# Kernel tuning notes

Hardware: AMD Instinct MI355X
Metric: run time of the kernel (lower is better)

Reference implementation:

```python
import jax, jax.numpy as jnp
import numpy as np
from jax import lax

FPS_NUM, K = 2048, 32


def fps_subsample(x, n):
    # x: [B, N, 3] -> [B, n, 3]; farthest point sampling, deterministic start at index 0
    B, N, _ = x.shape
    d0 = jnp.sum((x - x[:, :1]) ** 2, axis=-1)  # [B, N] dist to point 0

    def step(dists, _):
        nxt = jnp.argmax(dists, axis=1)                       # [B]
        p = x[jnp.arange(B), nxt]                             # [B, 3]
        dists = jnp.minimum(dists, jnp.sum((x - p[:, None]) ** 2, axis=-1))
        return dists, nxt

    _, idxs = lax.scan(step, d0, None, length=n - 1)          # [n-1, B]
    idxs = jnp.concatenate([jnp.zeros((1, B), jnp.int32), idxs.astype(jnp.int32)], axis=0).T  # [B, n]
    return x[jnp.arange(B)[:, None], idxs]                    # [B, n, 3]


def knn_idx(x, k):
    # x: [B, C, N] -> [B, N, k] indices of k nearest neighbors in feature space
    xx = jnp.sum(x * x, axis=1)                               # [B, N]
    inner = jnp.einsum('bcn,bcm->bnm', x, x)
    neg_dist = 2.0 * inner - xx[:, :, None] - xx[:, None, :]  # -||xi-xj||^2
    return lax.top_k(neg_dist, k)[1]


def get_graph_feature(x, k):
    # DGCNN edge features: x [B, C, N] -> [B, 2C, N, k]
    B, C, N = x.shape
    idx = knn_idx(x, k)                                       # [B, N, k]
    xt = jnp.transpose(x, (0, 2, 1))                          # [B, N, C]
    nbr = xt[jnp.arange(B)[:, None, None], idx]               # [B, N, k, C]
    ctr = jnp.broadcast_to(xt[:, :, None], nbr.shape)
    feat = jnp.concatenate([nbr - ctr, ctr], axis=-1)         # [B, N, k, 2C]
    return jnp.transpose(feat, (0, 3, 1, 2))


def attention(xq, xk, pos, Wq, bq, Wk, bk, Wv, bv, Wp, bp):
    # positional attention over k neighbors: xq/xk [B, Cin, N, k], pos [B, 3, N] -> [B, dim, N]
    q = jnp.einsum('bcnk,dc->bdnk', xq, Wq) + bq[:, None, None]
    kk = jnp.einsum('bcnk,dc->bdnk', xk, Wk) + bk[:, None, None]
    v = jnp.einsum('bcnk,dc->bdnk', xk, Wv) + bv[:, None, None]
    p = jnp.einsum('bcn,dc->bdn', pos, Wp) + bp[:, None]      # [B, dim, N]
    dim = Wq.shape[0]
    logits = jnp.einsum('bdnk,bdnk->bnk', q, kk) / jnp.sqrt(jnp.float32(dim))
    attn = jax.nn.softmax(logits, axis=-1)                    # [B, N, k]
    return jnp.einsum('bnk,bdnk->bdn', attn, v + p[:, :, :, None])


def _layer_params(key, cin, dim):
    ks = jax.random.split(key, 4)
    s = 1.0 / np.sqrt(cin)
    return (jax.random.normal(ks[0], (dim, cin), jnp.float32) * s,
            jnp.zeros((dim,), jnp.float32),
            jax.random.normal(ks[1], (dim, cin), jnp.float32) * s,
            jnp.zeros((dim,), jnp.float32),
            jax.random.normal(ks[2], (dim, cin), jnp.float32) * s,
            jnp.zeros((dim,), jnp.float32),
            jax.random.normal(ks[3], (dim, 3), jnp.float32) * (1.0 / np.sqrt(3.0)),
            jnp.zeros((dim,), jnp.float32))


def setup_inputs() -> dict:
    key = jax.random.key(0)
    kx, k1, k2, k3 = jax.random.split(key, 4)
    x = jax.random.normal(kx, (8, 16384, 3), jnp.float32)
    out = {'x': x}
    for name, kk_, cin, dim in (('t1', k1, 6, 64), ('t2', k2, 128, 64), ('t3', k3, 128, 128)):
        Wq, bq, Wk, bk, Wv, bv, Wp, bp = _layer_params(kk_, cin, dim)
        out.update({f'{name}_Wq': Wq, f'{name}_bq': bq, f'{name}_Wk': Wk, f'{name}_bk': bk,
                    f'{name}_Wv': Wv, f'{name}_bv': bv, f'{name}_Wp': Wp, f'{name}_bp': bp})
    return out


def reference(x, t1_Wq, t1_bq, t1_Wk, t1_bk, t1_Wv, t1_bv, t1_Wp, t1_bp,
              t2_Wq, t2_bq, t2_Wk, t2_bk, t2_Wv, t2_bv, t2_Wp, t2_bp,
              t3_Wq, t3_bq, t3_Wk, t3_bk, t3_Wv, t3_bv, t3_Wp, t3_bp):
    partial = jnp.transpose(fps_subsample(x, FPS_NUM), (0, 2, 1))       # [B, 3, n]
    g = get_graph_feature(partial, K)                                    # [B, 6, n, k]
    x1 = attention(g, g, partial, t1_Wq, t1_bq, t1_Wk, t1_bk, t1_Wv, t1_bv, t1_Wp, t1_bp)  # [B, 64, n]
    g = get_graph_feature(x1, K)                                         # [B, 128, n, k]
    x2 = attention(g, g, partial, t2_Wq, t2_bq, t2_Wk, t2_bk, t2_Wv, t2_bv, t2_Wp, t2_bp)  # [B, 64, n]
    g = get_graph_feature(x2, K)                                         # [B, 128, n, k]
    x3 = attention(g, g, partial, t3_Wq, t3_bq, t3_Wk, t3_bk, t3_Wv, t3_bv, t3_Wp, t3_bp)  # [B, 128, n]
    feats = jnp.concatenate([x1, x2, x3], axis=1)                        # [B, 256, n]
    return jnp.concatenate([jnp.max(feats, axis=-1), jnp.mean(feats, axis=-1)], axis=1)    # [B, 512]
```

## Files before the change

kernel.cpp:

```cpp
#include <hip/hip_runtime.h>
#include <math.h>

#define NB 8
#define NIN 16384
#define NP 2048
#define KNN 32
#define TOTPTS (NB * NP)

#define NEG_INF (-__builtin_inff())
#define POS_INF (__builtin_inff())

__device__ __forceinline__ float2 pk_add(float2 a, float2 b) {
  float2 d;
  asm("v_pk_add_f32 %0, %1, %2" : "=v"(d) : "v"(a), "v"(b));
  return d;
}
__device__ __forceinline__ float2 pk_mul(float2 a, float2 b) {
  float2 d;
  asm("v_pk_mul_f32 %0, %1, %2" : "=v"(d) : "v"(a), "v"(b));
  return d;
}

#define DPP_F(old, v, C, RM) \
  __int_as_float(__builtin_amdgcn_update_dpp(__float_as_int(old), __float_as_int(v), C, RM, 0xf, false))
#define DPP_I(old, v, C, RM) \
  __builtin_amdgcn_update_dpp(old, v, C, RM, 0xf, false)

__device__ __forceinline__ float wave_max_f(float v) {
  v = fmaxf(v, DPP_F(NEG_INF, v, 0x111, 0xf));
  v = fmaxf(v, DPP_F(NEG_INF, v, 0x112, 0xf));
  v = fmaxf(v, DPP_F(NEG_INF, v, 0x114, 0xf));
  v = fmaxf(v, DPP_F(NEG_INF, v, 0x118, 0xf));
  v = fmaxf(v, DPP_F(NEG_INF, v, 0x142, 0xa));
  v = fmaxf(v, DPP_F(NEG_INF, v, 0x143, 0xc));
  return v;
}
__device__ __forceinline__ float wave_min_f(float v) {
  v = fminf(v, DPP_F(POS_INF, v, 0x111, 0xf));
  v = fminf(v, DPP_F(POS_INF, v, 0x112, 0xf));
  v = fminf(v, DPP_F(POS_INF, v, 0x114, 0xf));
  v = fminf(v, DPP_F(POS_INF, v, 0x118, 0xf));
  v = fminf(v, DPP_F(POS_INF, v, 0x142, 0xa));
  v = fminf(v, DPP_F(POS_INF, v, 0x143, 0xc));
  return v;
}
__device__ __forceinline__ int wave_min_i(int v) {
  v = min(v, DPP_I(0x7fffffff, v, 0x111, 0xf));
  v = min(v, DPP_I(0x7fffffff, v, 0x112, 0xf));
  v = min(v, DPP_I(0x7fffffff, v, 0x114, 0xf));
  v = min(v, DPP_I(0x7fffffff, v, 0x118, 0xf));
  v = min(v, DPP_I(0x7fffffff, v, 0x142, 0xa));
  v = min(v, DPP_I(0x7fffffff, v, 0x143, 0xc));
  return v;
}

template <int CTRL, int RMASK>
__device__ __forceinline__ void dpp_amax_step(float& bv, int& bi) {
  float ov = DPP_F(NEG_INF, bv, CTRL, RMASK);
  int oi = DPP_I(0, bi, CTRL, RMASK);
  if (ov > bv || (ov == bv && oi < bi)) { bv = ov; bi = oi; }
}
__device__ __forceinline__ void wave_amax63(float& bv, int& bi) {
  dpp_amax_step<0x111, 0xf>(bv, bi);
  dpp_amax_step<0x112, 0xf>(bv, bi);
  dpp_amax_step<0x114, 0xf>(bv, bi);
  dpp_amax_step<0x118, 0xf>(bv, bi);
  dpp_amax_step<0x142, 0xa>(bv, bi);
  dpp_amax_step<0x143, 0xc>(bv, bi);
}

__device__ __forceinline__ float readlane63f(float v) {
  return __int_as_float(__builtin_amdgcn_readlane(__float_as_int(v), 63));
}

__device__ __forceinline__ unsigned f2ord(float f) {
  unsigned b = __float_as_uint(f);
  return (b & 0x80000000u) ? ~b : (b | 0x80000000u);
}
__device__ __forceinline__ float ord2f(unsigned u) {
  return __uint_as_float((u & 0x80000000u) ? (u ^ 0x80000000u) : ~u);
}
__device__ __forceinline__ unsigned spread3(unsigned v) {
  return (v & 1u) | ((v & 2u) << 2) | ((v & 4u) << 4) | ((v & 8u) << 6) |
         ((v & 16u) << 8) | ((v & 32u) << 10);
}

__global__ __launch_bounds__(1024) void sort_kernel(const float* __restrict__ x,
                                                    unsigned* __restrict__ ord) {
  const int b = blockIdx.x, t = threadIdx.x;
  const float* xb = x + (size_t)b * NIN * 3;
  __shared__ unsigned keys[NIN];
  __shared__ unsigned smn[3], smx[3];
  if (t < 3) { smn[t] = 0xFFFFFFFFu; smx[t] = 0u; }
  __syncthreads();
  float cx[16], cy[16], cz[16];
  float mnx = POS_INF, mny = POS_INF, mnz = POS_INF;
  float mxx = NEG_INF, mxy = NEG_INF, mxz = NEG_INF;
#pragma unroll
  for (int s = 0; s < 16; ++s) {
    const int i = s * 1024 + t;
    cx[s] = xb[3 * i]; cy[s] = xb[3 * i + 1]; cz[s] = xb[3 * i + 2];
    mnx = fminf(mnx, cx[s]); mxx = fmaxf(mxx, cx[s]);
    mny = fminf(mny, cy[s]); mxy = fmaxf(mxy, cy[s]);
    mnz = fminf(mnz, cz[s]); mxz = fmaxf(mxz, cz[s]);
  }
  mnx = wave_min_f(mnx); mxx = wave_max_f(mxx);
  mny = wave_min_f(mny); mxy = wave_max_f(mxy);
  mnz = wave_min_f(mnz); mxz = wave_max_f(mxz);
  if ((t & 63) == 63) {
    atomicMin(&smn[0], f2ord(mnx)); atomicMax(&smx[0], f2ord(mxx));
    atomicMin(&smn[1], f2ord(mny)); atomicMax(&smx[1], f2ord(mxy));
    atomicMin(&smn[2], f2ord(mnz)); atomicMax(&smx[2], f2ord(mxz));
  }
  __syncthreads();
  const float bx = ord2f(smn[0]), by = ord2f(smn[1]), bz = ord2f(smn[2]);
  const float fx = 63.9f / fmaxf(ord2f(smx[0]) - bx, 1e-30f);
  const float fy = 63.9f / fmaxf(ord2f(smx[1]) - by, 1e-30f);
  const float fz = 63.9f / fmaxf(ord2f(smx[2]) - bz, 1e-30f);
#pragma unroll
  for (int s = 0; s < 16; ++s) {
    const int i = s * 1024 + t;
    const unsigned a0 = min(63u, (unsigned)(int)fmaxf((cx[s] - bx) * fx, 0.f));
    const unsigned a1 = min(63u, (unsigned)(int)fmaxf((cy[s] - by) * fy, 0.f));
    const unsigned a2 = min(63u, (unsigned)(int)fmaxf((cz[s] - bz) * fz, 0.f));
    const unsigned code = spread3(a0) | (spread3(a1) << 1) | (spread3(a2) << 2);
    keys[i] = (code << 14) | (unsigned)i;
  }
  __syncthreads();
  for (unsigned k = 2; k <= (unsigned)NIN; k <<= 1) {
    for (unsigned j = k >> 1; j; j >>= 1) {
#pragma unroll
      for (int s = 0; s < 8; ++s) {
        const unsigned idx = (unsigned)t + (unsigned)s * 1024u;
        const unsigned e = ((idx & ~(j - 1u)) << 1) | (idx & (j - 1u));
        const unsigned p = e | j;
        const unsigned a = keys[e], c = keys[p];
        if ((a > c) == ((e & k) == 0u)) { keys[e] = c; keys[p] = a; }
      }
      __syncthreads();
    }
  }
#pragma unroll
  for (int s = 0; s < 16; ++s) {
    const int i = s * 1024 + t;
    ord[(size_t)b * NIN + i] = keys[i] & 0x3FFFu;
  }
}

#define FPS_UPD(j)                                                            \
  {                                                                           \
    float2 dx = pk_add(px[j], nx2), dy = pk_add(py[j], ny2), dz = pk_add(pz[j], nz2); \
    float2 nd = pk_add(pk_add(pk_mul(dx, dx), pk_mul(dy, dy)), pk_mul(dz, dz));        \
    dd[j].x = fminf(dd[j].x, nd.x);                                           \
    dd[j].y = fminf(dd[j].y, nd.y);                                           \
  }

__global__ __launch_bounds__(1024) void fps_kernel(const float* __restrict__ x,
                                                   const unsigned* __restrict__ ord,
                                                   float* __restrict__ partial) {
  const int b = blockIdx.x;
  const int t = threadIdx.x;
  const int w = t >> 6, l = t & 63;
  const float* xb = x + (size_t)b * NIN * 3;
  float* pb = partial + (size_t)b * NP * 3;
  __shared__ unsigned long long skey[NP];
  for (int i = t; i < NP; i += 1024) skey[i] = 0ull;

  float2 px[8], py[8], pz[8], dd[8];
  int id0[8], id1[8];
  const unsigned* ob = ord + (size_t)b * NIN;
#pragma unroll
  for (int j = 0; j < 8; ++j) {
    const int p0 = ((w * 8 + j) << 7) + l * 2;
    const int g0 = (int)ob[p0], g1 = (int)ob[p0 + 1];
    id0[j] = g0; id1[j] = g1;
    px[j] = make_float2(xb[3 * g0], xb[3 * g1]);
    py[j] = make_float2(xb[3 * g0 + 1], xb[3 * g1 + 1]);
    pz[j] = make_float2(xb[3 * g0 + 2], xb[3 * g1 + 2]);
  }

  float ccx = 0.f, ccy = 0.f, ccz = 0.f, ccr = 0.f;
#pragma unroll
  for (int j = 0; j < 8; ++j) {
    float mnx = wave_min_f(fminf(px[j].x, px[j].y));
    float mxx = wave_max_f(fmaxf(px[j].x, px[j].y));
    float mny = wave_min_f(fminf(py[j].x, py[j].y));
    float mxy = wave_max_f(fmaxf(py[j].x, py[j].y));
    float mnz = wave_min_f(fminf(pz[j].x, pz[j].y));
    float mxz = wave_max_f(fmaxf(pz[j].x, pz[j].y));
    const float cx = 0.5f * (readlane63f(mnx) + readlane63f(mxx));
    const float cy = 0.5f * (readlane63f(mny) + readlane63f(mxy));
    const float cz = 0.5f * (readlane63f(mnz) + readlane63f(mxz));
    float d0x = px[j].x - cx, d0y = py[j].x - cy, d0z = pz[j].x - cz;
    float d1x = px[j].y - cx, d1y = py[j].y - cy, d1z = pz[j].y - cz;
    float d2 = fmaxf(d0x * d0x + d0y * d0y + d0z * d0z,
                     d1x * d1x + d1y * d1y + d1z * d1z);
    d2 = wave_max_f(d2);
    const float r = sqrtf(readlane63f(d2)) * 1.00002f;
    if (l == j) { ccx = cx; ccy = cy; ccz = cz; ccr = r; }
  }

  const float qx0 = xb[0], qy0 = xb[1], qz0 = xb[2];
  if (t == 0) { pb[0] = qx0; pb[1] = qy0; pb[2] = qz0; }

  float bv = NEG_INF;
  int bi = 0x7fffffff;
  {
    const float2 nx2 = make_float2(-qx0, -qx0);
    const float2 ny2 = make_float2(-qy0, -qy0);
    const float2 nz2 = make_float2(-qz0, -qz0);
#pragma unroll
    for (int j = 0; j < 8; ++j) {
      float2 dx = pk_add(px[j], nx2), dy = pk_add(py[j], ny2), dz = pk_add(pz[j], nz2);
      float2 nd = pk_add(pk_add(pk_mul(dx, dx), pk_mul(dy, dy)), pk_mul(dz, dz));
      dd[j] = nd;
      if (nd.x > bv || (nd.x == bv && id0[j] < bi)) { bv = nd.x; bi = id0[j]; }
      if (nd.y > bv || (nd.y == bv && id1[j] < bi)) { bv = nd.y; bi = id1[j]; }
    }
  }
  __syncthreads();

  for (int it = 1; it < NP; ++it) {
    const float wm = wave_max_f(bv);
    const float smaxw = readlane63f(wm);
    const int sel = (bv == smaxw) ? bi : 0x7fffffff;
    const int wi = wave_min_i(sel);
    if (l == 63) {
      const unsigned long long key =
          ((unsigned long long)__float_as_uint(smaxw) << 32) | (unsigned)(~wi);
      atomicMax(&skey[it], key);
    }
    __syncthreads();
    const unsigned long long gk = skey[it];
    const float smax = __uint_as_float((unsigned)(gk >> 32));
    const int u = __builtin_amdgcn_readfirstlane((int)(~(unsigned)gk));
    const float nqx = xb[3 * u], nqy = xb[3 * u + 1], nqz = xb[3 * u + 2];
    if (t == 0) { pb[3 * it] = nqx; pb[3 * it + 1] = nqy; pb[3 * it + 2] = nqz; }

    const float rho = sqrtf(smax) * 1.00002f;
    const float cdx = ccx - nqx, cdy = ccy - nqy, cdz = ccz - nqz;
    const float dq = sqrtf(cdx * cdx + cdy * cdy + cdz * cdz);
    const bool upd = (l < 8) && (dq * 0.99998f < ccr + rho);
    const unsigned m8 = (unsigned)__ballot(upd) & 255u;
    if (m8) {
      const float2 nx2 = make_float2(-nqx, -nqx);
      const float2 ny2 = make_float2(-nqy, -nqy);
      const float2 nz2 = make_float2(-nqz, -nqz);
      if (m8 & 1u) FPS_UPD(0)
      if (m8 & 2u) FPS_UPD(1)
      if (m8 & 4u) FPS_UPD(2)
      if (m8 & 8u) FPS_UPD(3)
      if (m8 & 16u) FPS_UPD(4)
      if (m8 & 32u) FPS_UPD(5)
      if (m8 & 64u) FPS_UPD(6)
      if (m8 & 128u) FPS_UPD(7)
      bv = NEG_INF;
      bi = 0x7fffffff;
#pragma unroll
      for (int j = 0; j < 8; ++j) {
        if (dd[j].x > bv || (dd[j].x == bv && id0[j] < bi)) { bv = dd[j].x; bi = id0[j]; }
        if (dd[j].y > bv || (dd[j].y == bv && id1[j] < bi)) { bv = dd[j].y; bi = id1[j]; }
      }
    }
  }
}

__global__ void xx_kernel(const float* __restrict__ F, float* __restrict__ xxg, int C) {
  int i = blockIdx.x * 256 + threadIdx.x;
  if (i >= TOTPTS) return;
  const float* f = F + (size_t)i * C;
  float s = 0.f;
  for (int c = 0; c < C; ++c) s = __fadd_rn(s, __fmul_rn(f[c], f[c]));
  xxg[i] = s;
}

template <int C>
__global__ __launch_bounds__(256) void dist_gemm(const float* __restrict__ F,
                                                 const float* __restrict__ xxg,
                                                 float* __restrict__ D, int bofs) {
  __shared__ float As[64][C + 1];
  __shared__ float Bs[64][C + 1];
  const int b = bofs + blockIdx.z;
  float* Ds = D + (size_t)blockIdx.z * NP * NP;
  const int tid = threadIdx.x;
  const int n0 = blockIdx.y * 64, m0 = blockIdx.x * 64;
  const float* Fb = F + (size_t)b * NP * C;
  const float* xxb = xxg + b * NP;
  for (int t = tid; t < 64 * C; t += 256) {
    int r = t / C, c = t - r * C;
    As[r][c] = Fb[(size_t)(n0 + r) * C + c];
    Bs[r][c] = Fb[(size_t)(m0 + r) * C + c];
  }
  __syncthreads();
  const int tx = tid & 15, ty = tid >> 4;
  float acc[4][4] = {};
  for (int c = 0; c < C; ++c) {
    float a[4], bb[4];
#pragma unroll
    for (int i = 0; i < 4; ++i) a[i] = As[ty * 4 + i][c];
#pragma unroll
    for (int j = 0; j < 4; ++j) bb[j] = Bs[tx * 4 + j][c];
#pragma unroll
    for (int i = 0; i < 4; ++i)
#pragma unroll
      for (int j = 0; j < 4; ++j) acc[i][j] = fmaf(a[i], bb[j], acc[i][j]);
  }
#pragma unroll
  for (int i = 0; i < 4; ++i) {
    int n = n0 + ty * 4 + i;
    float xn = xxb[n];
    float4 o;
    o.x = __fsub_rn(__fsub_rn(2.0f * acc[i][0], xn), xxb[m0 + tx * 4 + 0]);
    o.y = __fsub_rn(__fsub_rn(2.0f * acc[i][1], xn), xxb[m0 + tx * 4 + 1]);
    o.z = __fsub_rn(__fsub_rn(2.0f * acc[i][2], xn), xxb[m0 + tx * 4 + 2]);
    o.w = __fsub_rn(__fsub_rn(2.0f * acc[i][3], xn), xxb[m0 + tx * 4 + 3]);
    *(float4*)&Ds[(size_t)n * NP + m0 + tx * 4] = o;
  }
}

__global__ __launch_bounds__(256) void select_kernel(const float* __restrict__ D,
                                                     int* __restrict__ idxg, int bofs) {
  const int lane = threadIdx.x & 63;
  const int b = bofs + blockIdx.z;
  const int row = blockIdx.x * 4 + (threadIdx.x >> 6);
  const float* Drow = D + (size_t)blockIdx.z * NP * NP + (size_t)row * NP;
  float v[32];
#pragma unroll
  for (int s = 0; s < 32; ++s) v[s] = Drow[s * 64 + lane];
  int* out = idxg + ((size_t)b * NP + row) * KNN;
  for (int t = 0; t < KNN; ++t) {
    float bv = v[0];
    int bs = 0;
#pragma unroll
    for (int s = 1; s < 32; ++s) {
      if (v[s] > bv) { bv = v[s]; bs = s; }
    }
    int bi = bs * 64 + lane;
    wave_amax63(bv, bi);
    const int wbi = __builtin_amdgcn_readlane(bi, 63);
    if (lane == 0) out[t] = wbi;
    const bool own = (lane == (wbi & 63));
    const int cs = wbi >> 6;
#pragma unroll
    for (int s = 0; s < 32; ++s)
      if (own && s == cs) v[s] = NEG_INF;
  }
}

template <int C, int DIM>
__global__ __launch_bounds__(256) void proj_kernel(
    const float* __restrict__ F, const float* __restrict__ pos,
    const float* __restrict__ Wq, const float* __restrict__ bq,
    const float* __restrict__ Wk, const float* __restrict__ bk,
    const float* __restrict__ Wv, const float* __restrict__ bv,
    const float* __restrict__ Wp, const float* __restrict__ bp,
    float* __restrict__ Uq, float* __restrict__ Uk, float* __restrict__ Uv,
    float* __restrict__ Uqc, float* __restrict__ Ukc, float* __restrict__ W6) {
  constexpr int PTS = 16;
  constexpr int GROUPS = 256 / DIM;
  constexpr int PPT = PTS / GROUPS;
  __shared__ float xs[PTS][C];
  __shared__ float ps[PTS][3];
  const int tid = threadIdx.x;
  const int base = blockIdx.x * PTS;
  for (int t = tid; t < PTS * C; t += 256) {
    int r = t / C;
    xs[r][t - r * C] = F[(size_t)(base + r) * C + (t - r * C)];
  }
  for (int t = tid; t < PTS * 3; t += 256) {
    int r = t / 3;
    ps[r][t - r * 3] = pos[(size_t)(base + r) * 3 + (t - r * 3)];
  }
  __syncthreads();
  const int g = tid / DIM;
  const int d = tid - g * DIM;
  float uq[PPT], uqd[PPT], uk[PPT], ukd[PPT], uv[PPT], uvd[PPT];
#pragma unroll
  for (int p = 0; p < PPT; ++p) { uq[p] = uqd[p] = uk[p] = ukd[p] = uv[p] = uvd[p] = 0.f; }
  const float* wqr = Wq + (size_t)d * (2 * C);
  const float* wkr = Wk + (size_t)d * (2 * C);
  const float* wvr = Wv + (size_t)d * (2 * C);
  for (int c = 0; c < C; ++c) {
    const float wq1 = wqr[c], wqd_ = wqr[C + c] - wq1;
    const float wk1 = wkr[c], wkd_ = wkr[C + c] - wk1;
    const float wv1 = wvr[c], wvd_ = wvr[C + c] - wv1;
#pragma unroll
    for (int p = 0; p < PPT; ++p) {
      const float xc = xs[g + p * GROUPS][c];
      uq[p] = fmaf(wq1, xc, uq[p]);
      uqd[p] = fmaf(wqd_, xc, uqd[p]);
      uk[p] = fmaf(wk1, xc, uk[p]);
      ukd[p] = fmaf(wkd_, xc, ukd[p]);
      uv[p] = fmaf(wv1, xc, uv[p]);
      uvd[p] = fmaf(wvd_, xc, uvd[p]);
    }
  }
  const float bqd = bq[d], bkd = bk[d], bvd = bv[d];
  const float wp0 = Wp[d * 3], wp1 = Wp[d * 3 + 1], wp2 = Wp[d * 3 + 2], bpd = bp[d];
#pragma unroll
  for (int p = 0; p < PPT; ++p) {
    const int lp = g + p * GROUPS;
    const size_t o = (size_t)(base + lp) * DIM + d;
    const float pd = wp0 * ps[lp][0] + wp1 * ps[lp][1] + wp2 * ps[lp][2] + bpd;
    Uq[o] = uq[p];
    Uqc[o] = uqd[p] + bqd;
    Uk[o] = uk[p];
    Ukc[o] = ukd[p] + bkd;
    Uv[o] = uv[p];
    W6[o] = uvd[p] + bvd + pd;
  }
}

template <int DIM>
__global__ void prep_kernel(const float* __restrict__ Wq, const float* __restrict__ bq,
                            const float* __restrict__ Wk, const float* __restrict__ bk,
                            const float* __restrict__ Wv, const float* __restrict__ bv,
                            float* __restrict__ Wcat, float* __restrict__ bcat) {
  const int o = blockIdx.x * 256 + threadIdx.x;
  constexpr int ND = 6 * DIM;
  if (o >= ND) return;
  const int blk = o / DIM, d = o % DIM;
  bcat[o] = (blk == 1) ? bq[d] : (blk == 3) ? bk[d] : (blk == 5) ? bv[d] : 0.f;
  const float* W = (blk < 2) ? Wq : (blk < 4) ? Wk : Wv;
  for (int c = 0; c < 64; ++c) {
    const float w1 = W[(size_t)d * 128 + c];
    const float w2 = W[(size_t)d * 128 + 64 + c];
    Wcat[(size_t)c * ND + o] = (blk & 1) ? (w2 - w1) : w1;
  }
}

template <int DIM>
__global__ void pos_kernel(const float* __restrict__ pos, const float* __restrict__ Wp,
                           const float* __restrict__ bp, float* __restrict__ P) {
  const int idx = blockIdx.x * 256 + threadIdx.x;
  const int pt = idx / DIM, d = idx - pt * DIM;
  P[idx] = Wp[d * 3] * pos[pt * 3] + Wp[d * 3 + 1] * pos[pt * 3 + 1] +
           Wp[d * 3 + 2] * pos[pt * 3 + 2] + bp[d];
}

template <int DIM>
__global__ __launch_bounds__(256) void gemm_proj(
    const float* __restrict__ F, const float* __restrict__ Wcat,
    const float* __restrict__ bcat, const float* __restrict__ P,
    float* __restrict__ Uq, float* __restrict__ Uqc, float* __restrict__ Uk,
    float* __restrict__ Ukc, float* __restrict__ Uv, float* __restrict__ W6) {
  constexpr int ND = 6 * DIM;
  __shared__ float As[64][65];
  __shared__ float Bs[64][65];
  const int tid = threadIdx.x;
  const int p0 = blockIdx.x * 64;
  const int n0 = blockIdx.y * 64;
  {
    const int r0 = tid >> 4, c4 = (tid & 15) * 4;
    for (int r = r0; r < 64; r += 16) {
      float4 a = *(const float4*)&F[(size_t)(p0 + r) * 64 + c4];
      As[r][c4] = a.x; As[r][c4 + 1] = a.y; As[r][c4 + 2] = a.z; As[r][c4 + 3] = a.w;
      float4 bb = *(const float4*)&Wcat[(size_t)r * ND + n0 + c4];
      Bs[r][c4] = bb.x; Bs[r][c4 + 1] = bb.y; Bs[r][c4 + 2] = bb.z; Bs[r][c4 + 3] = bb.w;
    }
  }
  __syncthreads();
  const int tx = tid & 15, ty = tid >> 4;
  float acc[4][4] = {};
#pragma unroll 4
  for (int c = 0; c < 64; ++c) {
    float a[4], bb[4];
#pragma unroll
    for (int i = 0; i < 4; ++i) a[i] = As[ty * 4 + i][c];
#pragma unroll
    for (int j = 0; j < 4; ++j) bb[j] = Bs[c][tx * 4 + j];
#pragma unroll
    for (int i = 0; i < 4; ++i)
#pragma unroll
      for (int j = 0; j < 4; ++j) acc[i][j] = fmaf(a[i], bb[j], acc[i][j]);
  }
  const int obuf = n0 / DIM;
  const int oloc = n0 - obuf * DIM;
  float* outp = (obuf == 0) ? Uq : (obuf == 1) ? Uqc : (obuf == 2) ? Uk
              : (obuf == 3) ? Ukc : (obuf == 4) ? Uv : W6;
  const float b0 = bcat[n0 + tx * 4], b1 = bcat[n0 + tx * 4 + 1];
  const float b2 = bcat[n0 + tx * 4 + 2], b3 = bcat[n0 + tx * 4 + 3];
#pragma unroll
  for (int i = 0; i < 4; ++i) {
    const int p = p0 + ty * 4 + i;
    float4 r = make_float4(acc[i][0] + b0, acc[i][1] + b1, acc[i][2] + b2, acc[i][3] + b3);
    if (obuf == 5) {
      float4 pv = *(const float4*)&P[(size_t)p * DIM + oloc + tx * 4];
      r.x += pv.x; r.y += pv.y; r.z += pv.z; r.w += pv.w;
    }
    *(float4*)&outp[(size_t)p * DIM + oloc + tx * 4] = r;
  }
}

template <int DIM>
__global__ __launch_bounds__(256) void attn_kernel(
    const float* __restrict__ Uq, const float* __restrict__ Uk, const float* __restrict__ Uv,
    const float* __restrict__ Uqc, const float* __restrict__ Ukc, const float* __restrict__ W6g,
    const int* __restrict__ idxg, float* __restrict__ outF) {
  const int w = threadIdx.x >> 6, lane = threadIdx.x & 63;
  const int pt = blockIdx.x * 4 + w;
  const int b = pt >> 11;
  __shared__ int sidx[4][KNN];
  __shared__ float sqc[4][DIM], skc[4][DIM], sw6[4][DIM];
  __shared__ float sattn[4][KNN];
  const size_t rowo = (size_t)pt * DIM;
  if (lane < KNN) sidx[w][lane] = idxg[(size_t)pt * KNN + lane];
  for (int d = lane; d < DIM; d += 64) {
    sqc[w][d] = Uqc[rowo + d];
    skc[w][d] = Ukc[rowo + d];
    sw6[w][d] = W6g[rowo + d];
  }
  __syncthreads();
  {
    const int kk = lane & 31;
    const int h = lane >> 5;
    const int ik = sidx[w][kk];
    const float* qr = Uq + (size_t)(b * NP + ik) * DIM;
    const float* kr = Uk + (size_t)(b * NP + ik) * DIM;
    float lg = 0.f;
    const int d0 = h * (DIM / 2), d1 = d0 + DIM / 2;
    for (int d = d0; d < d1; d += 4) {
      float4 qa = *(const float4*)(qr + d);
      float4 ka = *(const float4*)(kr + d);
      float4 qc = *(const float4*)(&sqc[w][d]);
      float4 kc = *(const float4*)(&skc[w][d]);
      lg += (qa.x + qc.x) * (ka.x + kc.x);
      lg += (qa.y + qc.y) * (ka.y + kc.y);
      lg += (qa.z + qc.z) * (ka.z + kc.z);
      lg += (qa.w + qc.w) * (ka.w + kc.w);
    }
    lg += __shfl_xor(lg, 32);
    lg *= (DIM == 64) ? 0.125f : 0.08838834764831845f;
    float m = lg;
#pragma unroll
    for (int off = 16; off; off >>= 1) m = fmaxf(m, __shfl_xor(m, off));
    float e = expf(lg - m);
    float s = e;
#pragma unroll
    for (int off = 16; off; off >>= 1) s += __shfl_xor(s, off);
    if (lane < KNN) sattn[w][lane] = e / s;
  }
  __syncthreads();
  float acc[DIM / 64];
#pragma unroll
  for (int q = 0; q < DIM / 64; ++q) acc[q] = 0.f;
  for (int k = 0; k < KNN; ++k) {
    const int ik = sidx[w][k];
    const float a = sattn[w][k];
    const float* vr = Uv + (size_t)(b * NP + ik) * DIM;
#pragma unroll
    for (int q = 0; q < DIM / 64; ++q) {
      const int d = q * 64 + lane;
      acc[q] = fmaf(a, vr[d] + sw6[w][d], acc[q]);
    }
  }
#pragma unroll
  for (int q = 0; q < DIM / 64; ++q) outF[rowo + q * 64 + lane] = acc[q];
}

__global__ __launch_bounds__(256) void pool_kernel(const float* __restrict__ x1,
                                                   const float* __restrict__ x2,
                                                   const float* __restrict__ x3,
                                                   float* __restrict__ out) {
  const int b = blockIdx.x, c = threadIdx.x;
  const float* src;
  int dim, cl;
  if (c < 64) {
    src = x1 + (size_t)b * NP * 64; dim = 64; cl = c;
  } else if (c < 128) {
    src = x2 + (size_t)b * NP * 64; dim = 64; cl = c - 64;
  } else {
    src = x3 + (size_t)b * NP * 128; dim = 128; cl = c - 128;
  }
  float mx = NEG_INF, sm = 0.f;
#pragma unroll 8
  for (int n = 0; n < NP; ++n) {
    float v = src[(size_t)n * dim + cl];
    mx = fmaxf(mx, v);
    sm += v;
  }
  out[b * 512 + c] = mx;
  out[b * 512 + 256 + c] = sm * (1.0f / 2048.0f);
}

extern "C" void kernel_launch(void* const* d_in, const int* in_sizes, int n_in,
                              void* d_out, int out_size, void* d_ws, size_t ws_size,
                              hipStream_t stream) {
  const float* x = (const float*)d_in[0];
  const float* W[24];
  for (int i = 0; i < 24; ++i) W[i] = (const float*)d_in[1 + i];

  float* ws = (float*)d_ws;
  size_t off = 0;
  float* partial = ws + off; off += (size_t)NB * NP * 3;
  float* xxbuf = ws + off;   off += TOTPTS;
  int* idxb = (int*)(ws + off); off += (size_t)TOTPTS * KNN;
  unsigned* ordb = (unsigned*)(ws + off); off += (size_t)NB * NIN;
  float* x1 = ws + off; off += (size_t)TOTPTS * 64;
  float* x2 = ws + off; off += (size_t)TOTPTS * 64;
  float* x3 = ws + off; off += (size_t)TOTPTS * 128;
  float* Uq = ws + off;  off += (size_t)TOTPTS * 128;
  float* Uk = ws + off;  off += (size_t)TOTPTS * 128;
  float* Uv = ws + off;  off += (size_t)TOTPTS * 128;
  float* Uqc = ws + off; off += (size_t)TOTPTS * 128;
  float* Ukc = ws + off; off += (size_t)TOTPTS * 128;
  float* W6 = ws + off;  off += (size_t)TOTPTS * 128;
  float* Pbuf = ws + off; off += (size_t)TOTPTS * 128;
  float* Wcat = ws + off; off += (size_t)64 * 768;
  float* bcat = ws + off; off += 768;
  if (ws_size < off * sizeof(float)) return;

  float* Dbig = ws + off;
  const size_t need_big = (off + (size_t)NB * NP * NP) * sizeof(float);
  const bool bigws = (ws_size >= need_big);
  float* D = bigws ? Dbig : Uq;
  const int NZ = bigws ? NB : 1;

  sort_kernel<<<NB, 1024, 0, stream>>>(x, ordb);
  fps_kernel<<<NB, 1024, 0, stream>>>(x, ordb, partial);

  xx_kernel<<<TOTPTS / 256, 256, 0, stream>>>(partial, xxbuf, 3);
  for (int b = 0; b < NB; b += NZ) {
    dist_gemm<3><<<dim3(32, 32, NZ), 256, 0, stream>>>(partial, xxbuf, D, b);
    select_kernel<<<dim3(NP / 4, 1, NZ), 256, 0, stream>>>(D, idxb, b);
  }
  proj_kernel<3, 64><<<TOTPTS / 16, 256, 0, stream>>>(
      partial, partial, W[0], W[1], W[2], W[3], W[4], W[5], W[6], W[7],
      Uq, Uk, Uv, Uqc, Ukc, W6);
  attn_kernel<64><<<TOTPTS / 4, 256, 0, stream>>>(Uq, Uk, Uv, Uqc, Ukc, W6, idxb, x1);

  xx_kernel<<<TOTPTS / 256, 256, 0, stream>>>(x1, xxbuf, 64);
  for (int b = 0; b < NB; b += NZ) {
    dist_gemm<64><<<dim3(32, 32, NZ), 256, 0, stream>>>(x1, xxbuf, D, b);
    select_kernel<<<dim3(NP / 4, 1, NZ), 256, 0, stream>>>(D, idxb, b);
  }
  prep_kernel<64><<<2, 256, 0, stream>>>(W[8], W[9], W[10], W[11], W[12], W[13], Wcat, bcat);
  pos_kernel<64><<<TOTPTS * 64 / 256, 256, 0, stream>>>(partial, W[14], W[15], Pbuf);
  gemm_proj<64><<<dim3(TOTPTS / 64, 6), 256, 0, stream>>>(
      x1, Wcat, bcat, Pbuf, Uq, Uqc, Uk, Ukc, Uv, W6);
  attn_kernel<64><<<TOTPTS / 4, 256, 0, stream>>>(Uq, Uk, Uv, Uqc, Ukc, W6, idxb, x2);

  xx_kernel<<<TOTPTS / 256, 256, 0, stream>>>(x2, xxbuf, 64);
  for (int b = 0; b < NB; b += NZ) {
    dist_gemm<64><<<dim3(32, 32, NZ), 256, 0, stream>>>(x2, xxbuf, D, b);
    select_kernel<<<dim3(NP / 4, 1, NZ), 256, 0, stream>>>(D, idxb, b);
  }
  prep_kernel<128><<<3, 256, 0, stream>>>(W[16], W[17], W[18], W[19], W[20], W[21], Wcat, bcat);
  pos_kernel<128><<<TOTPTS * 128 / 256, 256, 0, stream>>>(partial, W[22], W[23], Pbuf);
  gemm_proj<128><<<dim3(TOTPTS / 64, 12), 256, 0, stream>>>(
      x2, Wcat, bcat, Pbuf, Uq, Uqc, Uk, Ukc, Uv, W6);
  attn_kernel<128><<<TOTPTS / 4, 256, 0, stream>>>(Uq, Uk, Uv, Uqc, Ukc, W6, idxb, x3);

  pool_kernel<<<NB, 256, 0, stream>>>(x1, x2, x3, (float*)d_out);
}
```

Measured before the change: 5.240 ms.

## Keep per-chunk max distances in shared memory and reduce them redundantly per wave

The FPS loop now stores, for each of the 128 spatial chunks, its current max distance, index and coordinates in shared memory. Every wave then reduces those 128 candidates itself, which replaces the per-wave reduction, the 64-bit atomicMax and the global-memory coordinate fetch of the winning point. Only chunks that were updated recompute their record. This costs a second __syncthreads per iteration in exchange for a shorter serial dependency chain in each of the 2047 FPS steps.

```diff
diff --git a/kernel.cpp b/kernel.cpp
--- a/kernel.cpp
+++ b/kernel.cpp
@@ -44,20 +44,11 @@
   v = fminf(v, DPP_F(POS_INF, v, 0x143, 0xc));
   return v;
 }
-__device__ __forceinline__ int wave_min_i(int v) {
-  v = min(v, DPP_I(0x7fffffff, v, 0x111, 0xf));
-  v = min(v, DPP_I(0x7fffffff, v, 0x112, 0xf));
-  v = min(v, DPP_I(0x7fffffff, v, 0x114, 0xf));
-  v = min(v, DPP_I(0x7fffffff, v, 0x118, 0xf));
-  v = min(v, DPP_I(0x7fffffff, v, 0x142, 0xa));
-  v = min(v, DPP_I(0x7fffffff, v, 0x143, 0xc));
-  return v;
-}
 
 template <int CTRL, int RMASK>
 __device__ __forceinline__ void dpp_amax_step(float& bv, int& bi) {
   float ov = DPP_F(NEG_INF, bv, CTRL, RMASK);
-  int oi = DPP_I(0, bi, CTRL, RMASK);
+  int oi = DPP_I(0x7fffffff, bi, CTRL, RMASK);
   if (ov > bv || (ov == bv && oi < bi)) { bv = ov; bi = oi; }
 }
 __device__ __forceinline__ void wave_amax63(float& bv, int& bi) {
@@ -155,6 +146,20 @@
     dd[j].y = fminf(dd[j].y, nd.y);                                           \
   }
 
+#define FPS_RECORD(j)                                                         \
+  {                                                                           \
+    float bv2 = dd[j].x;                                                      \
+    int bi2 = id0[j];                                                         \
+    if (dd[j].y > bv2 || (dd[j].y == bv2 && id1[j] < bi2)) { bv2 = dd[j].y; bi2 = id1[j]; } \
+    wave_amax63(bv2, bi2);                                                    \
+    const float cv = readlane63f(bv2);                                        \
+    const int ci = __builtin_amdgcn_readlane(bi2, 63);                        \
+    const int c = w * 8 + (j);                                                \
+    if (l == 63) { cdist[c] = cv; cidx[c] = ci; }                             \
+    if (id0[j] == ci) { ccox[c] = px[j].x; ccoy[c] = py[j].x; ccoz[c] = pz[j].x; } \
+    if (id1[j] == ci) { ccox[c] = px[j].y; ccoy[c] = py[j].y; ccoz[c] = pz[j].y; } \
+  }
+
 __global__ __launch_bounds__(1024) void fps_kernel(const float* __restrict__ x,
                                                    const unsigned* __restrict__ ord,
                                                    float* __restrict__ partial) {
@@ -163,8 +168,9 @@
   const int w = t >> 6, l = t & 63;
   const float* xb = x + (size_t)b * NIN * 3;
   float* pb = partial + (size_t)b * NP * 3;
-  __shared__ unsigned long long skey[NP];
-  for (int i = t; i < NP; i += 1024) skey[i] = 0ull;
+  __shared__ float cdist[128];
+  __shared__ int cidx[128];
+  __shared__ float ccox[128], ccoy[128], ccoz[128];
 
   float2 px[8], py[8], pz[8], dd[8];
   int id0[8], id1[8];
@@ -203,8 +209,6 @@
   const float qx0 = xb[0], qy0 = xb[1], qz0 = xb[2];
   if (t == 0) { pb[0] = qx0; pb[1] = qy0; pb[2] = qz0; }
 
-  float bv = NEG_INF;
-  int bi = 0x7fffffff;
   {
     const float2 nx2 = make_float2(-qx0, -qx0);
     const float2 ny2 = make_float2(-qy0, -qy0);
@@ -212,29 +216,28 @@
 #pragma unroll
     for (int j = 0; j < 8; ++j) {
       float2 dx = pk_add(px[j], nx2), dy = pk_add(py[j], ny2), dz = pk_add(pz[j], nz2);
-      float2 nd = pk_add(pk_add(pk_mul(dx, dx), pk_mul(dy, dy)), pk_mul(dz, dz));
-      dd[j] = nd;
-      if (nd.x > bv || (nd.x == bv && id0[j] < bi)) { bv = nd.x; bi = id0[j]; }
-      if (nd.y > bv || (nd.y == bv && id1[j] < bi)) { bv = nd.y; bi = id1[j]; }
-    }
+      dd[j] = pk_add(pk_add(pk_mul(dx, dx), pk_mul(dy, dy)), pk_mul(dz, dz));
+    }
+#pragma unroll
+    for (int j = 0; j < 8; ++j) FPS_RECORD(j)
   }
   __syncthreads();
 
   for (int it = 1; it < NP; ++it) {
-    const float wm = wave_max_f(bv);
-    const float smaxw = readlane63f(wm);
-    const int sel = (bv == smaxw) ? bi : 0x7fffffff;
-    const int wi = wave_min_i(sel);
-    if (l == 63) {
-      const unsigned long long key =
-          ((unsigned long long)__float_as_uint(smaxw) << 32) | (unsigned)(~wi);
-      atomicMax(&skey[it], key);
-    }
-    __syncthreads();
-    const unsigned long long gk = skey[it];
-    const float smax = __uint_as_float((unsigned)(gk >> 32));
-    const int u = __builtin_amdgcn_readfirstlane((int)(~(unsigned)gk));
-    const float nqx = xb[3 * u], nqy = xb[3 * u + 1], nqz = xb[3 * u + 2];
+    const float d0 = cdist[l], d1 = cdist[64 + l];
+    const int i0c = cidx[l], i1c = cidx[64 + l];
+    float bv = d0;
+    int bi = i0c;
+    if (d1 > bv || (d1 == bv && i1c < bi)) { bv = d1; bi = i1c; }
+    wave_amax63(bv, bi);
+    const float smax = readlane63f(bv);
+    const int wi = __builtin_amdgcn_readlane(bi, 63);
+    const bool own0 = (i0c == wi), own1 = (i1c == wi);
+    const unsigned long long mask = __ballot(own0 || own1);
+    const int lsrc = (int)__builtin_ctzll(mask);
+    const int h = __builtin_amdgcn_readlane(own1 ? 1 : 0, lsrc);
+    const int cstar = lsrc + (h ? 64 : 0);
+    const float nqx = ccox[cstar], nqy = ccoy[cstar], nqz = ccoz[cstar];
     if (t == 0) { pb[3 * it] = nqx; pb[3 * it + 1] = nqy; pb[3 * it + 2] = nqz; }
 
     const float rho = sqrtf(smax) * 1.00002f;
@@ -242,6 +245,7 @@
     const float dq = sqrtf(cdx * cdx + cdy * cdy + cdz * cdz);
     const bool upd = (l < 8) && (dq * 0.99998f < ccr + rho);
     const unsigned m8 = (unsigned)__ballot(upd) & 255u;
+
     if (m8) {
       const float2 nx2 = make_float2(-nqx, -nqx);
       const float2 ny2 = make_float2(-nqy, -nqy);
@@ -254,14 +258,19 @@
       if (m8 & 32u) FPS_UPD(5)
       if (m8 & 64u) FPS_UPD(6)
       if (m8 & 128u) FPS_UPD(7)
-      bv = NEG_INF;
-      bi = 0x7fffffff;
-#pragma unroll
-      for (int j = 0; j < 8; ++j) {
-        if (dd[j].x > bv || (dd[j].x == bv && id0[j] < bi)) { bv = dd[j].x; bi = id0[j]; }
-        if (dd[j].y > bv || (dd[j].y == bv && id1[j] < bi)) { bv = dd[j].y; bi = id1[j]; }
-      }
-    }
+    }
+    __syncthreads();
+    if (m8) {
+      if (m8 & 1u) FPS_RECORD(0)
+      if (m8 & 2u) FPS_RECORD(1)
+      if (m8 & 4u) FPS_RECORD(2)
+      if (m8 & 8u) FPS_RECORD(3)
+      if (m8 & 16u) FPS_RECORD(4)
+      if (m8 & 32u) FPS_RECORD(5)
+      if (m8 & 64u) FPS_RECORD(6)
+      if (m8 & 128u) FPS_RECORD(7)
+    }
+    __syncthreads();
   }
 }
 
```

Measured after the change: 9.648 ms. +84.1%, slower.

## Replace FPS atomic key reduction with double-buffered per-wave candidate table

Applied to the files above, without the earlier changes.

Each wave now computes its own argmax candidate with a fused value/index DPP reduction and publishes its value, index and coordinates to a small double-buffered shared table. After a single barrier, every wave reduces the 16 entries itself and reads the winning coordinates from shared memory. This removes the shared-memory atomicMax, the separate min-index reduction and the dependent global load of the selected point on every iteration. Waves whose distances are unchanged reuse their cached candidate. The cost is extra readlane and ballot work, more registers, and the added sbest coordinate-selection logic.

```diff
diff --git a/kernel.cpp b/kernel.cpp
--- a/kernel.cpp
+++ b/kernel.cpp
@@ -44,20 +44,11 @@
   v = fminf(v, DPP_F(POS_INF, v, 0x143, 0xc));
   return v;
 }
-__device__ __forceinline__ int wave_min_i(int v) {
-  v = min(v, DPP_I(0x7fffffff, v, 0x111, 0xf));
-  v = min(v, DPP_I(0x7fffffff, v, 0x112, 0xf));
-  v = min(v, DPP_I(0x7fffffff, v, 0x114, 0xf));
-  v = min(v, DPP_I(0x7fffffff, v, 0x118, 0xf));
-  v = min(v, DPP_I(0x7fffffff, v, 0x142, 0xa));
-  v = min(v, DPP_I(0x7fffffff, v, 0x143, 0xc));
-  return v;
-}
 
 template <int CTRL, int RMASK>
 __device__ __forceinline__ void dpp_amax_step(float& bv, int& bi) {
   float ov = DPP_F(NEG_INF, bv, CTRL, RMASK);
-  int oi = DPP_I(0, bi, CTRL, RMASK);
+  int oi = DPP_I(0x7fffffff, bi, CTRL, RMASK);
   if (ov > bv || (ov == bv && oi < bi)) { bv = ov; bi = oi; }
 }
 __device__ __forceinline__ void wave_amax63(float& bv, int& bi) {
@@ -71,6 +62,9 @@
 
 __device__ __forceinline__ float readlane63f(float v) {
   return __int_as_float(__builtin_amdgcn_readlane(__float_as_int(v), 63));
+}
+__device__ __forceinline__ float readlanef(float v, int l) {
+  return __int_as_float(__builtin_amdgcn_readlane(__float_as_int(v), l));
 }
 
 __device__ __forceinline__ unsigned f2ord(float f) {
@@ -155,6 +149,25 @@
     dd[j].y = fminf(dd[j].y, nd.y);                                           \
   }
 
+#define FPS_CANDIDATE                                                         \
+  {                                                                           \
+    float rv = bv; int ri = bi;                                               \
+    wave_amax63(rv, ri);                                                      \
+    cwv = readlane63f(rv);                                                    \
+    cwi = __builtin_amdgcn_readlane(ri, 63);                                  \
+    float ax = px[0].x, ay = py[0].x, az = pz[0].x;                           \
+    _Pragma("unroll")                                                         \
+    for (int j = 0; j < 8; ++j) {                                             \
+      if (sbest == 2 * j)     { ax = px[j].x; ay = py[j].x; az = pz[j].x; }   \
+      if (sbest == 2 * j + 1) { ax = px[j].y; ay = py[j].y; az = pz[j].y; }   \
+    }                                                                         \
+    const unsigned long long ownm = __ballot(bv == cwv && bi == cwi);         \
+    const int lsrc = (int)__builtin_ctzll(ownm);                              \
+    wcx = readlanef(ax, lsrc);                                                \
+    wcy = readlanef(ay, lsrc);                                                \
+    wcz = readlanef(az, lsrc);                                                \
+  }
+
 __global__ __launch_bounds__(1024) void fps_kernel(const float* __restrict__ x,
                                                    const unsigned* __restrict__ ord,
                                                    float* __restrict__ partial) {
@@ -163,8 +176,9 @@
   const int w = t >> 6, l = t & 63;
   const float* xb = x + (size_t)b * NIN * 3;
   float* pb = partial + (size_t)b * NP * 3;
-  __shared__ unsigned long long skey[NP];
-  for (int i = t; i < NP; i += 1024) skey[i] = 0ull;
+  __shared__ float sval[2][16];
+  __shared__ int sidw[2][16];
+  __shared__ float slx[2][16], sly[2][16], slz[2][16];
 
   float2 px[8], py[8], pz[8], dd[8];
   int id0[8], id1[8];
@@ -179,7 +193,7 @@
     pz[j] = make_float2(xb[3 * g0 + 2], xb[3 * g1 + 2]);
   }
 
-  float ccx = 0.f, ccy = 0.f, ccz = 0.f, ccr = 0.f;
+  float gcx = 0.f, gcy = 0.f, gcz = 0.f, gcr = 0.f;
 #pragma unroll
   for (int j = 0; j < 8; ++j) {
     float mnx = wave_min_f(fminf(px[j].x, px[j].y));
@@ -197,7 +211,7 @@
                      d1x * d1x + d1y * d1y + d1z * d1z);
     d2 = wave_max_f(d2);
     const float r = sqrtf(readlane63f(d2)) * 1.00002f;
-    if (l == j) { ccx = cx; ccy = cy; ccz = cz; ccr = r; }
+    if (l == j) { gcx = cx; gcy = cy; gcz = cz; gcr = r; }
   }
 
   const float qx0 = xb[0], qy0 = xb[1], qz0 = xb[2];
@@ -205,6 +219,7 @@
 
   float bv = NEG_INF;
   int bi = 0x7fffffff;
+  int sbest = 0;
   {
     const float2 nx2 = make_float2(-qx0, -qx0);
     const float2 ny2 = make_float2(-qy0, -qy0);
@@ -214,34 +229,43 @@
       float2 dx = pk_add(px[j], nx2), dy = pk_add(py[j], ny2), dz = pk_add(pz[j], nz2);
       float2 nd = pk_add(pk_add(pk_mul(dx, dx), pk_mul(dy, dy)), pk_mul(dz, dz));
       dd[j] = nd;
-      if (nd.x > bv || (nd.x == bv && id0[j] < bi)) { bv = nd.x; bi = id0[j]; }
-      if (nd.y > bv || (nd.y == bv && id1[j] < bi)) { bv = nd.y; bi = id1[j]; }
-    }
-  }
-  __syncthreads();
-
+      if (nd.x > bv || (nd.x == bv && id0[j] < bi)) { bv = nd.x; bi = id0[j]; sbest = 2 * j; }
+      if (nd.y > bv || (nd.y == bv && id1[j] < bi)) { bv = nd.y; bi = id1[j]; sbest = 2 * j + 1; }
+    }
+  }
+  float cwv, wcx, wcy, wcz;
+  int cwi;
+  FPS_CANDIDATE
+  if (l == 0) {
+    sval[0][w] = cwv; sidw[0][w] = cwi;
+    slx[0][w] = wcx; sly[0][w] = wcy; slz[0][w] = wcz;
+  }
+  __syncthreads();
+
+  int cur = 0;
   for (int it = 1; it < NP; ++it) {
-    const float wm = wave_max_f(bv);
-    const float smaxw = readlane63f(wm);
-    const int sel = (bv == smaxw) ? bi : 0x7fffffff;
-    const int wi = wave_min_i(sel);
-    if (l == 63) {
-      const unsigned long long key =
-          ((unsigned long long)__float_as_uint(smaxw) << 32) | (unsigned)(~wi);
-      atomicMax(&skey[it], key);
-    }
-    __syncthreads();
-    const unsigned long long gk = skey[it];
-    const float smax = __uint_as_float((unsigned)(gk >> 32));
-    const int u = __builtin_amdgcn_readfirstlane((int)(~(unsigned)gk));
-    const float nqx = xb[3 * u], nqy = xb[3 * u + 1], nqz = xb[3 * u + 2];
+    const int s = l & 15;
+    const float v0 = sval[cur][s];
+    const int i0 = sidw[cur][s];
+    float rv = v0;
+    int ri = i0;
+    dpp_amax_step<0x111, 0xf>(rv, ri);
+    dpp_amax_step<0x112, 0xf>(rv, ri);
+    dpp_amax_step<0x114, 0xf>(rv, ri);
+    dpp_amax_step<0x118, 0xf>(rv, ri);
+    const float smax = readlane63f(rv);
+    const int wi = __builtin_amdgcn_readlane(ri, 63);
+    const unsigned long long wm = __ballot(v0 == smax && i0 == wi);
+    const int sstar = (int)__builtin_ctzll(wm);
+    const float nqx = slx[cur][sstar], nqy = sly[cur][sstar], nqz = slz[cur][sstar];
     if (t == 0) { pb[3 * it] = nqx; pb[3 * it + 1] = nqy; pb[3 * it + 2] = nqz; }
 
     const float rho = sqrtf(smax) * 1.00002f;
-    const float cdx = ccx - nqx, cdy = ccy - nqy, cdz = ccz - nqz;
+    const float cdx = gcx - nqx, cdy = gcy - nqy, cdz = gcz - nqz;
     const float dq = sqrtf(cdx * cdx + cdy * cdy + cdz * cdz);
-    const bool upd = (l < 8) && (dq * 0.99998f < ccr + rho);
+    const bool upd = (l < 8) && (dq * 0.99998f < gcr + rho);
     const unsigned m8 = (unsigned)__ballot(upd) & 255u;
+    const int nxt = cur ^ 1;
     if (m8) {
       const float2 nx2 = make_float2(-nqx, -nqx);
       const float2 ny2 = make_float2(-nqy, -nqy);
@@ -256,12 +280,20 @@
       if (m8 & 128u) FPS_UPD(7)
       bv = NEG_INF;
       bi = 0x7fffffff;
+      sbest = 0;
 #pragma unroll
       for (int j = 0; j < 8; ++j) {
-        if (dd[j].x > bv || (dd[j].x == bv && id0[j] < bi)) { bv = dd[j].x; bi = id0[j]; }
-        if (dd[j].y > bv || (dd[j].y == bv && id1[j] < bi)) { bv = dd[j].y; bi = id1[j]; }
+        if (dd[j].x > bv || (dd[j].x == bv && id0[j] < bi)) { bv = dd[j].x; bi = id0[j]; sbest = 2 * j; }
+        if (dd[j].y > bv || (dd[j].y == bv && id1[j] < bi)) { bv = dd[j].y; bi = id1[j]; sbest = 2 * j + 1; }
       }
-    }
+      FPS_CANDIDATE
+    }
+    if (l == 0) {
+      sval[nxt][w] = cwv; sidw[nxt][w] = cwi;
+      slx[nxt][w] = wcx; sly[nxt][w] = wcy; slz[nxt][w] = wcz;
+    }
+    cur = nxt;
+    __syncthreads();
   }
 }
 
```

After: 7.552 ms. 1.44x slower.
